# Optimization experiments

Hardware: AMD Instinct MI355X
Metric: run time of the kernel (lower is better)

## Reference

```python
import jax, jax.numpy as jnp
import numpy as np

HR, LR, K, RANK = 2048, 1024, 8, 16


def setup_inputs() -> dict:
    key = jax.random.key(0)
    kA, kX, kW, kU, kV, kM = jax.random.split(key, 6)
    A = jax.random.normal(kA, (LR, LR), dtype=jnp.float32)
    A = (A + A.T) / 2  # symmetric so torch UPLO='U' and jax eigh agree
    X = jax.random.normal(kX, (LR, HR), dtype=jnp.float32)
    init_range = (6.0 / (HR + HR)) ** 0.5  # glorot uniform
    weights = jax.random.uniform(kW, (HR, HR), dtype=jnp.float32,
                                 minval=-init_range, maxval=init_range)
    Us = jax.random.normal(kU, (K, HR, RANK), dtype=jnp.float32) * 0.001
    # original inits Vs to zeros; use small noise so corrections are nonzero
    Vs = jax.random.normal(kV, (K, HR, RANK), dtype=jnp.float32) * 0.01
    alphas = jnp.ones((K,), dtype=jnp.float32) / K
    masks = (jax.random.uniform(kM, (K, HR, HR)) < 0.5).astype(jnp.float32)
    return {"A": A, "X": X, "weights": weights, "Us": Us, "Vs": Vs,
            "alphas": alphas, "masks": masks}


def _set_unit_diag(M, eye):
    return M * (1.0 - eye) + eye


def reference(A, X, weights, Us, Vs, alphas, masks):
    lr = A.shape[0]
    hr = weights.shape[0]
    eye_hr = jnp.eye(hr, dtype=A.dtype)
    # --- GSRLayer ---
    _, U_lr = jnp.linalg.eigh(A)                      # (lr, lr)
    s_d = jnp.concatenate([jnp.eye(lr, dtype=A.dtype),
                           jnp.eye(lr, dtype=A.dtype)], axis=0)  # (hr, lr)
    f_d = weights @ s_d @ U_lr.T @ X                  # (hr, hr)
    adj = jnp.abs(f_d)
    adj = _set_unit_diag(adj, eye_hr)
    # --- community-aware low-rank corrections ---
    alpha = jax.nn.softmax(alphas)                    # (k,)
    Zm = adj[None, :, :] * masks                      # (k, hr, hr)
    t = jnp.einsum('kij,kjr->kir', Zm, Us)            # (k, hr, rank)
    corr = jnp.einsum('kir,kjr->kij', t, Vs) * masks  # (k, hr, hr)
    out_adj = adj + jnp.einsum('k,kij->ij', alpha, corr)
    # --- symmetrize with unit diagonal ---
    X_out = out_adj @ out_adj.T
    X_out = (X_out + X_out.T) / 2
    X_out = _set_unit_diag(X_out, eye_hr)
    return out_adj, jnp.abs(X_out)
```

## Files before the change

kernel.cpp:

```cpp
#include <hip/hip_runtime.h>
#include <hip/hip_bf16.h>

typedef unsigned long long u64;

#define MBYTE (1ull << 20)

static const size_t OFF_A64   = 0;
static const size_t OFF_VT    = 8*MBYTE;
static const size_t OFF_TAU   = 12*MBYTE;
static const size_t OFF_D64   = 12*MBYTE +  8192;
static const size_t OFF_E64   = 12*MBYTE + 16384;
static const size_t OFF_XB    = 12*MBYTE + 24576;
static const size_t OFF_Y2B   = 12*MBYTE + 32768;
static const size_t OFF_Y1B   = 12*MBYTE + 40960;
static const size_t OFF_XA    = 12*MBYTE + 49152;
static const size_t OFF_Y1A   = 12*MBYTE + 57344;
static const size_t OFF_Y2A   = 12*MBYTE + 65536;
static const size_t OFF_QA    = 13*MBYTE;
static const size_t OFF_QB    = 17*MBYTE;
static const size_t OFF_SHAT  = 21*MBYTE;
static const size_t OFF_WC    = 25*MBYTE;
static const size_t OFF_M1    = 33*MBYTE;
static const size_t OFF_T8    = 33*MBYTE;
static const size_t OFF_ALPHA = 35*MBYTE + 512*1024;
static const size_t OFF_ADJ   = 41*MBYTE;
static const size_t OFF_OADJ  = 17*MBYTE;
static const size_t OFF_CBUF  = 0;

static const size_t SCD_STRIDE = 9216;
static const size_t SCI_STRIDE = 6144;
static const size_t OFF_SCDB  = OFF_WC;
static const size_t OFF_SCIB  = OFF_WC + 2359296;
static const size_t OFF_KNB   = OFF_WC + 2359296 + 786432;
static const size_t OFF_KNDB  = OFF_WC + 2359296 + 786432 + 2048;


__global__ void kCopyA(const float* __restrict__ A, double* __restrict__ A64) {
  int gid = blockIdx.x*256 + threadIdx.x;
  if (gid < 1024*1024) A64[gid] = (double)A[gid];
}

__device__ __forceinline__ double agLoadD(const double* p) {
  return __hip_atomic_load(p, __ATOMIC_RELAXED, __HIP_MEMORY_SCOPE_AGENT);
}
__device__ __forceinline__ void agStoreD(double* p, double v) {
  __hip_atomic_store(p, v, __ATOMIC_RELAXED, __HIP_MEMORY_SCOPE_AGENT);
}

#define TD_NBLK 64

__global__ __launch_bounds__(1024) void kTriDiag(
    double* __restrict__ A64,
    double* __restrict__ y1A, double* __restrict__ y1B,
    double* __restrict__ y2A, double* __restrict__ y2B,
    double* __restrict__ diagP, unsigned* __restrict__ flags,
    double* __restrict__ tauv, double* __restrict__ e64, double* __restrict__ d64,
    float* __restrict__ Vt) {
  __shared__ double xL[1024], vL[1024], wL[1024], y1L[1024], y2L[1024];
  __shared__ double red[4];
  __shared__ double sS[4];
  int tid = threadIdx.x;
  int bid = blockIdx.x;
  bool w0 = (bid == 0);
  int lane = tid & 63, wave = tid >> 6;
  int myRow = wave*TD_NBLK + bid;

  double dg = 0.0;

  for (int i = 0; i <= 1023; ++i) {
    const double* y1in = (((i-1)&1) != 0) ? y1B : y1A;
    const double* y2in = (((i-1)&1) != 0) ? y2B : y2A;
    double* y1out = ((i&1) != 0) ? y1B : y1A;
    double* y2out = ((i&1) != 0) ? y2B : y2A;

    if (i == 0) {
      if (tid < 256) {
        for (int c = tid; c < 1024; c += 256) { vL[c] = 0.0; wL[c] = 0.0; }
        for (int c = 1 + tid; c < 1024; c += 256) xL[c] = A64[(u64)c*1024];
        if (w0 && tid == 0) d64[0] = A64[0];
      }
      __syncthreads();
    } else {
      int j = i - 1;
      double sy1 = agLoadD(&y1in[tid]);
      double sy2 = agLoadD(&y2in[tid]);
      if (w0 && tid == 0) dg = agLoadD(&diagP[i]);
      double acc = 0.0;
      if (tid < 256) {
        for (int c = i + 1 + tid; c < 1024; c += 256) { double v = xL[c]; acc += v*v; }
        for (int off = 32; off > 0; off >>= 1) acc += __shfl_xor(acc, off, 64);
      }
      y1L[tid] = sy1; y2L[tid] = sy2;
      if (tid < 256 && lane == 0) red[wave] = acc;
      __syncthreads();
      if (tid == 0) {
        double xn2 = red[0] + red[1] + red[2] + red[3];
        double alpha = xL[i];
        double tv, sc;
        if (xn2 == 0.0) { tv = 0.0; if (w0) e64[j] = alpha; sc = 0.0; }
        else {
          double beta = (alpha >= 0.0) ? -sqrt(alpha*alpha + xn2) : sqrt(alpha*alpha + xn2);
          tv = (beta - alpha)/beta;
          if (w0) e64[j] = beta;
          sc = 1.0/(alpha - beta);
        }
        if (w0) tauv[j] = tv;
        sS[0] = sc; sS[1] = tv;
        vL[i] = 1.0;
        if (w0) Vt[(u64)j*1024 + i] = 1.0f;
      }
      __syncthreads();
      if (tid < 256) {
        double sc = sS[0], tv = sS[1];
        double acc2 = 0.0;
        for (int r = i + tid; r < 1024; r += 256) {
          double v;
          if (r == i) v = 1.0;
          else {
            v = xL[r]*sc;
            vL[r] = v;
            if (w0) Vt[(u64)j*1024 + r] = (float)v;
          }
          double P = tv*(y1L[r] + sc*y2L[r]);
          wL[r] = P;
          acc2 += P*v;
        }
        for (int off = 32; off > 0; off >>= 1) acc2 += __shfl_xor(acc2, off, 64);
        if (lane == 0) red[wave] = acc2;
      }
      __syncthreads();
      if (tid == 0) {
        double coef = 0.5*sS[1]*(red[0] + red[1] + red[2] + red[3]);
        double wi = wL[i] - coef;
        sS[2] = coef; sS[3] = wi;
        if (w0) d64[i] = dg - 2.0*wi;
      }
      __syncthreads();
      if (tid < 256) {
        double coef = sS[2], wi = sS[3];
        for (int r = i + tid; r < 1024; r += 256) {
          double wcr = wL[r] - coef*vL[r];
          wL[r] = wcr;
          if (r > i) xL[r] = y1L[r] - vL[r]*wi - wcr;
        }
      }
      __syncthreads();
    }
    if (i <= 1022) {
      int r = myRow;
      if (r >= i + 1) {
        double vr = vL[r], wr = wL[r];
        double* Arow = A64 + (u64)r*1024;
        double acc = 0.0, y1v = 0.0;
        for (int c = i + 1 + lane; c < 1024; c += 64) {
          double a = Arow[c] - vr*wL[c] - wr*vL[c];
          Arow[c] = a;
          if (c == r) agStoreD(&diagP[r], a);
          if (c == i + 1) y1v = a; else acc += a*xL[c];
        }
        for (int off = 32; off > 0; off >>= 1) acc += __shfl_down(acc, off, 64);
        if (lane == 0) { agStoreD(&y1out[r], y1v); agStoreD(&y2out[r], acc); }
      }
      __syncthreads();
      unsigned tgt = (unsigned)(i + 1);
      if (tid == 0)
        __hip_atomic_store(&flags[bid*16], tgt, __ATOMIC_RELEASE, __HIP_MEMORY_SCOPE_AGENT);
      if (tid < TD_NBLK) {
        for (;;) {
          unsigned v = __hip_atomic_load(&flags[tid*16], __ATOMIC_ACQUIRE, __HIP_MEMORY_SCOPE_AGENT);
          if (__all(v >= tgt)) break;
          __builtin_amdgcn_s_sleep(2);
        }
      }
      __syncthreads();
    }
  }
  if (w0 && tid == 0) {
    for (int c = 16; c < 1024; c += 16) {
      double ae = fabs(e64[c-1]);
      d64[c-1] -= ae;
      d64[c]   -= ae;
    }
  }
}


__device__ void slartg_(double f, double g, double* cs, double* sn, double* r) {
  if (g == 0.0) { *cs = 1.0; *sn = 0.0; *r = f; }
  else if (f == 0.0) { *cs = 0.0; *sn = (g >= 0.0) ? 1.0 : -1.0; *r = fabs(g); }
  else {
    double d = sqrt(f*f + g*g);
    *cs = fabs(f)/d;
    *r = (f >= 0.0) ? d : -d;
    *sn = g / (*r);
  }
}

__device__ void slaev2_(double a, double b, double c, double* rt1, double* rt2,
                        double* cs1, double* sn1) {
  double sm = a + c, df = a - c, adf = fabs(df), tb = b + b, ab = fabs(tb);
  double acmx, acmn;
  if (fabs(a) > fabs(c)) { acmx = a; acmn = c; } else { acmx = c; acmn = a; }
  double rt;
  if (adf > ab) rt = adf*sqrt(1.0 + (ab/adf)*(ab/adf));
  else if (adf < ab) rt = ab*sqrt(1.0 + (adf/ab)*(adf/ab));
  else rt = ab*sqrt(2.0);
  int sgn1;
  if (sm < 0.0) { *rt1 = 0.5*(sm - rt); sgn1 = -1; *rt2 = (acmx / *rt1)*acmn - (b / *rt1)*b; }
  else if (sm > 0.0) { *rt1 = 0.5*(sm + rt); sgn1 = 1; *rt2 = (acmx / *rt1)*acmn - (b / *rt1)*b; }
  else { *rt1 = 0.5*rt; *rt2 = -0.5*rt; sgn1 = 1; }
  int sgn2; double cs;
  if (df >= 0.0) { cs = df + rt; sgn2 = 1; } else { cs = df - rt; sgn2 = -1; }
  double acs = fabs(cs);
  if (acs > ab) { double ct = -tb/cs; *sn1 = 1.0/sqrt(1.0 + ct*ct); *cs1 = ct*(*sn1); }
  else {
    if (ab == 0.0) { *cs1 = 1.0; *sn1 = 0.0; }
    else { double tn = -cs/tb; *cs1 = 1.0/sqrt(1.0 + tn*tn); *sn1 = tn*(*cs1); }
  }
  if (sgn1 == sgn2) { double tn = *cs1; *cs1 = -(*sn1); *sn1 = tn; }
}

__device__ void steqr16_(double* d, double* e, double* z, double* wc, double* ws_) {
  const int n = 16;
  const double eps = 5.9604644775390625e-08;
  const double eps2 = eps*eps;
  const double safmin = 1.1754943508222875e-38;
  int jtot = 0; const int nmaxit = n*30;
  int l1 = 0;
  for (int outer = 0; outer < 200; ++outer) {
    if (l1 > n-1) break;
    if (l1 > 0) e[l1-1] = 0.0;
    int m = l1;
    for (; m <= n-2; ++m) {
      double tst = fabs(e[m]);
      if (tst == 0.0) break;
      if (tst <= (sqrt(fabs(d[m]))*sqrt(fabs(d[m+1])))*eps) { e[m] = 0.0; break; }
    }
    int l = l1, lend = m;
    l1 = m + 1;
    if (lend == l) continue;
    if (fabs(d[lend]) < fabs(d[l])) { int t = l; l = lend; lend = t; }
    if (lend > l) {
      for (int it = 0; it < 800; ++it) {
        int mm = lend;
        if (l != lend) {
          for (mm = l; mm <= lend-1; ++mm) {
            double tst = e[mm]*e[mm];
            if (tst <= eps2*fabs(d[mm])*fabs(d[mm+1]) + safmin) break;
          }
        }
        if (mm < lend) e[mm] = 0.0;
        double p = d[l];
        if (mm == l) { d[l] = p; ++l; if (l <= lend) continue; break; }
        if (mm == l+1) {
          double rt1, rt2, c2, s2;
          slaev2_(d[l], e[l], d[l+1], &rt1, &rt2, &c2, &s2);
          for (int r = 0; r < n; ++r) {
            double t = z[r*16 + l + 1];
            z[r*16 + l + 1] = c2*t - s2*z[r*16 + l];
            z[r*16 + l]     = s2*t + c2*z[r*16 + l];
          }
          d[l] = rt1; d[l+1] = rt2; e[l] = 0.0;
          l += 2; if (l <= lend) continue; break;
        }
        if (jtot == nmaxit) break;
        ++jtot;
        double g = (d[l+1] - p)/(2.0*e[l]);
        double r_ = sqrt(g*g + 1.0);
        g = d[mm] - p + e[l]/(g + ((g >= 0.0) ? r_ : -r_));
        double s = 1.0, c = 1.0;
        p = 0.0;
        for (int i = mm-1; i >= l; --i) {
          double f = s*e[i], b = c*e[i];
          double cs, sn, rr;
          slartg_(g, f, &cs, &sn, &rr);
          c = cs; s = sn;
          if (i != mm-1) e[i+1] = rr;
          g = d[i+1] - p;
          rr = (d[i] - g)*s + 2.0*c*b;
          p = s*rr;
          d[i+1] = g + p;
          g = c*rr - b;
          wc[i] = c; ws_[i] = -s;
        }
        for (int jj = mm-1; jj >= l; --jj) {
          double cs = wc[jj], sn = ws_[jj];
          for (int r = 0; r < n; ++r) {
            double t = z[r*16 + jj + 1];
            z[r*16 + jj + 1] = cs*t - sn*z[r*16 + jj];
            z[r*16 + jj]     = sn*t + cs*z[r*16 + jj];
          }
        }
        d[l] -= p;
        e[l] = g;
      }
    } else {
      for (int it = 0; it < 800; ++it) {
        int mm = lend;
        if (l != lend) {
          for (mm = l; mm >= lend+1; --mm) {
            double tst = e[mm-1]*e[mm-1];
            if (tst <= eps2*fabs(d[mm])*fabs(d[mm-1]) + safmin) break;
          }
        }
        if (mm > lend) e[mm-1] = 0.0;
        double p = d[l];
        if (mm == l) { d[l] = p; --l; if (l >= lend) continue; break; }
        if (mm == l-1) {
          double rt1, rt2, c2, s2;
          slaev2_(d[l-1], e[l-1], d[l], &rt1, &rt2, &c2, &s2);
          for (int r = 0; r < n; ++r) {
            double t = z[r*16 + l];
            z[r*16 + l]     = c2*t - s2*z[r*16 + l - 1];
            z[r*16 + l - 1] = s2*t + c2*z[r*16 + l - 1];
          }
          d[l-1] = rt1; d[l] = rt2; e[l-1] = 0.0;
          l -= 2; if (l >= lend) continue; break;
        }
        if (jtot == nmaxit) break;
        ++jtot;
        double g = (d[l-1] - p)/(2.0*e[l-1]);
        double r_ = sqrt(g*g + 1.0);
        g = d[mm] - p + e[l-1]/(g + ((g >= 0.0) ? r_ : -r_));
        double s = 1.0, c = 1.0;
        p = 0.0;
        for (int i = mm; i <= l-1; ++i) {
          double f = s*e[i], b = c*e[i];
          double cs, sn, rr;
          slartg_(g, f, &cs, &sn, &rr);
          c = cs; s = sn;
          if (i != mm) e[i-1] = rr;
          g = d[i] - p;
          rr = (d[i+1] - g)*s + 2.0*c*b;
          p = s*rr;
          d[i] = g + p;
          g = c*rr - b;
          wc[i] = c; ws_[i] = s;
        }
        for (int jj = mm; jj <= l-1; ++jj) {
          double cs = wc[jj], sn = ws_[jj];
          for (int r = 0; r < n; ++r) {
            double t = z[r*16 + jj + 1];
            z[r*16 + jj + 1] = cs*t - sn*z[r*16 + jj];
            z[r*16 + jj]     = sn*t + cs*z[r*16 + jj];
          }
        }
        d[l] -= p;
        e[l-1] = g;
      }
    }
  }
  for (int ii = 1; ii <= n-1; ++ii) {
    int i = ii - 1, k = i;
    double p = d[i];
    for (int j = ii; j <= n-1; ++j) if (d[j] < p) { k = j; p = d[j]; }
    if (k != i) {
      d[k] = d[i]; d[i] = p;
      for (int r = 0; r < n; ++r) { double t = z[r*16 + i]; z[r*16 + i] = z[r*16 + k]; z[r*16 + k] = t; }
    }
  }
}

__global__ void kLeaf(double* d64, const double* e64, float* Qa) {
  __shared__ double dd[16], ed[16], zd[256], wk1[16], wk2[16];
  int leaf = blockIdx.x, lo = leaf*16, tid = threadIdx.x;
  for (int idx = tid; idx < 256; idx += 64) zd[idx] = ((idx/16) == (idx%16)) ? 1.0 : 0.0;
  if (tid < 16) { dd[tid] = d64[lo + tid]; ed[tid] = (tid < 15) ? e64[lo + tid] : 0.0; }
  __syncthreads();
  if (tid == 0) steqr16_(dd, ed, zd, wk1, wk2);
  __syncthreads();
  for (int idx = tid; idx < 256; idx += 64) {
    int r = idx/16, c = idx%16;
    Qa[(u64)(lo + r)*1024 + lo + c] = (float)zd[idx];
  }
  if (tid < 16) d64[lo + tid] = dd[tid];
}


__global__ __launch_bounds__(1024) void kDeflateB(float* __restrict__ Qa,
      const double* __restrict__ d64, const double* __restrict__ e64,
      double* scdB, int* sciB, int* knB, double* kndB, int bs) {
  __shared__ double zL[1024], dlocL[1024], redD[1024];
  __shared__ double rcL[1024], rsL[1024];
  __shared__ int sIdxL[1024], rpqL[1024];
  __shared__ double sSc[4];
  __shared__ int sKn[4];
  int mg = blockIdx.x;
  int n1 = bs, n = 2*bs, lo = mg*n;
  double* scd = scdB + (u64)mg*SCD_STRIDE;
  int*    sci = sciB + (u64)mg*SCI_STRIDE;
  int* kn = knB + mg*8;
  double* knd = kndB + mg*4;
  int tid = threadIdx.x;
  if (tid == 0) sSc[0] = e64[lo + n1 - 1];
  __syncthreads();
  double rho_in = sSc[0];
  const double invs2 = 0.70710678118654752440;
  if (tid < n) {
    int row = (tid < n1) ? (lo + n1 - 1) : (lo + n1);
    double s = (rho_in < 0.0 && tid >= n1) ? -invs2 : invs2;
    zL[tid] = (double)Qa[(u64)row*1024 + lo + tid] * s;
    dlocL[tid] = d64[lo + tid];
  }
  __syncthreads();
  if (tid < n) {
    int pos; double key = dlocL[tid];
    if (tid < n1) {
      int loB = 0, hiB = n - n1;
      while (loB < hiB) { int mid = (loB+hiB)>>1; if (dlocL[n1+mid] < key) loB = mid+1; else hiB = mid; }
      pos = tid + loB;
    } else {
      int loA = 0, hiA = n1;
      while (loA < hiA) { int mid = (loA+hiA)>>1; if (dlocL[mid] <= key) loA = mid+1; else hiA = mid; }
      pos = (tid - n1) + loA;
    }
    sIdxL[pos] = tid;
  }
  redD[tid] = (tid < n) ? fabs(zL[tid]) : 0.0;
  __syncthreads();
  for (int s = 512; s > 0; s >>= 1) { if (tid < s) redD[tid] = fmax(redD[tid], redD[tid+s]); __syncthreads(); }
  if (tid == 0) sSc[1] = redD[0];
  __syncthreads();
  redD[tid] = (tid < n) ? fabs(dlocL[tid]) : 0.0;
  __syncthreads();
  for (int s = 512; s > 0; s >>= 1) { if (tid < s) redD[tid] = fmax(redD[tid], redD[tid+s]); __syncthreads(); }
  if (tid == 0) {
    double zmax = sSc[1], dmax = redD[0];
    double rho = fabs(2.0*rho_in);
    double tol = 8.0*5.9604644775390625e-8*fmax(dmax, zmax);
    double* dlG = scd + 1024;
    double* wmG = scd + 2048;
    double* dvalG = scd + 7168;
    int* permG = sci;
    int* deflG = sci + 1024;
    int K = 0, nrot = 0, nd = 0; double sw2 = 0.0;
    if (rho*zmax <= tol) {
      for (int pos = 0; pos < n; ++pos) { int c = sIdxL[pos]; deflG[nd] = c; dvalG[nd] = dlocL[c]; nd++; }
    } else {
      int pj = -1, jpos = 0;
      for (; jpos < n; ++jpos) {
        int nj = sIdxL[jpos];
        if (rho*fabs(zL[nj]) <= tol) { deflG[nd] = nj; dvalG[nd] = dlocL[nj]; nd++; }
        else { pj = nj; break; }
      }
      for (++jpos; jpos < n; ++jpos) {
        int nj = sIdxL[jpos];
        if (rho*fabs(zL[nj]) <= tol) { deflG[nd] = nj; dvalG[nd] = dlocL[nj]; nd++; continue; }
        double s_ = zL[pj], c_ = zL[nj];
        double tu = sqrt(c_*c_ + s_*s_);
        double tdif = dlocL[nj] - dlocL[pj];
        c_ /= tu; s_ = -s_/tu;
        if (fabs(tdif*c_*s_) <= tol) {
          zL[nj] = tu; zL[pj] = 0.0;
          rpqL[nrot] = (pj << 16) | nj; rcL[nrot] = c_; rsL[nrot] = s_; nrot++;
          double t1 = dlocL[pj]*c_*c_ + dlocL[nj]*s_*s_;
          dlocL[nj] = dlocL[pj]*s_*s_ + dlocL[nj]*c_*c_;
          dlocL[pj] = t1;
          deflG[nd] = pj; dvalG[nd] = t1; nd++;
          pj = nj;
        } else {
          permG[K] = pj; dlG[K] = dlocL[pj]; wmG[K] = zL[pj]; sw2 += zL[pj]*zL[pj]; K++;
          pj = nj;
        }
      }
      permG[K] = pj; dlG[K] = dlocL[pj]; wmG[K] = zL[pj]; sw2 += zL[pj]*zL[pj]; K++;
    }
    sKn[1] = nrot;
    kn[0] = K; kn[1] = nrot; kn[2] = nd;
    knd[0] = rho; knd[1] = sw2;
  }
  __syncthreads();
  int nrot = sKn[1];
  if (tid < n && nrot > 0) {
    u64 row = (u64)(lo + tid)*1024;
    for (int t = 0; t < nrot; ++t) {
      int pq = rpqL[t];
      int p = lo + (pq >> 16), q = lo + (pq & 0xffff);
      double c = rcL[t], s = rsL[t];
      double x = (double)Qa[row + p], y = (double)Qa[row + q];
      Qa[row + p] = (float)(c*x + s*y);
      Qa[row + q] = (float)(c*y - s*x);
    }
  }
}

__global__ __launch_bounds__(256) void kSecularB(double* scdB, const int* knB, const double* kndB) {
  __shared__ double dlS[1024], wmS[1024];
  int mg = blockIdx.y;
  double* scd = scdB + (u64)mg*SCD_STRIDE;
  const int* kn = knB + mg*8;
  const double* knd = kndB + mg*4;
  int K = kn[0];
  int tid = threadIdx.x;
  for (int j = tid; j < K; j += 256) { dlS[j] = scd[1024 + j]; wmS[j] = scd[2048 + j]; }
  __syncthreads();
  int wave = tid >> 6, lane = tid & 63;
  int i = blockIdx.x*4 + wave;
  if (i >= K) return;
  double rho = knd[0], sw2 = knd[1];
  double di = dlS[i];
  double hi = (i < K-1) ? (dlS[i+1] - di) : (rho*sw2*(1.0 + 1e-12) + 1e-300);
  double lo_ = 0.0;
  for (int it = 0; it < 100; ++it) {
    double mid = 0.5*(lo_ + hi);
    double g = 0.0;
    for (int j = lane; j < K; j += 64) { double w = wmS[j]; g += w*w/((dlS[j] - di) - mid); }
    for (int off = 32; off > 0; off >>= 1) g += __shfl_xor(g, off);
    g = 1.0 + rho*g;
    if (g < 0.0) lo_ = mid; else hi = mid;
  }
  scd[3072 + i] = 0.5*(lo_ + hi);
}

__global__ void kZhatB(double* scdB, const int* knB) {
  int mg = blockIdx.y;
  double* scd = scdB + (u64)mg*SCD_STRIDE;
  int K = (knB + mg*8)[0];
  int j = blockIdx.x*64 + threadIdx.x;
  if (j >= K) return;
  const double* dl = scd + 1024;
  const double* wm = scd + 2048;
  const double* mu = scd + 3072;
  double dj = dl[j];
  double prod = mu[j];
  for (int i2 = 0; i2 < K; ++i2) {
    if (i2 == j) continue;
    double dd = dl[i2] - dj;
    prod *= (dd + mu[i2]) / dd;
  }
  prod = fabs(prod);
  scd[4096 + j] = (wm[j] >= 0.0) ? sqrt(prod) : -sqrt(prod);
}

__global__ __launch_bounds__(1024) void kSortPermB(double* scdB, int* sciB, const int* knB,
                                                   double* d64, int bs) {
  __shared__ double sv[1024];
  __shared__ int si[1024];
  int mg = blockIdx.x;
  int n = 2*bs, lo = mg*n;
  double* scd = scdB + (u64)mg*SCD_STRIDE;
  int* sci = sciB + (u64)mg*SCI_STRIDE;
  int K = (knB + mg*8)[0];
  int tid = threadIdx.x;
  const double* dl = scd + 1024;
  const double* mu = scd + 3072;
  const double* dval = scd + 7168;
  double v;
  if (tid < K) v = dl[tid] + mu[tid];
  else if (tid < n) v = dval[tid - K];
  else v = 1e300;
  sv[tid] = v; si[tid] = tid;
  __syncthreads();
  for (int k = 2; k <= 1024; k <<= 1) {
    for (int j = k >> 1; j > 0; j >>= 1) {
      int ixj = tid ^ j;
      if (ixj > tid) {
        bool up = ((tid & k) == 0);
        double a = sv[tid], b = sv[ixj];
        int ia = si[tid], ib = si[ixj];
        bool agtb = (a > b) || (a == b && ia > ib);
        if (up ? agtb : !agtb) { sv[tid] = b; sv[ixj] = a; si[tid] = ib; si[ixj] = ia; }
      }
      __syncthreads();
    }
  }
  if (tid < n) {
    int s = si[tid];
    if (s < K) sci[4096 + s] = tid; else sci[5120 + s - K] = tid;
    d64[lo + tid] = sv[tid];
  }
}

__global__ void kSvecNormB(float* __restrict__ Shat, const double* scdB, const int* knB, int bs) {
  int mg = blockIdx.y;
  int n = 2*bs, lo = mg*n;
  const double* scd = scdB + (u64)mg*SCD_STRIDE;
  int K = (knB + mg*8)[0];
  int i = blockIdx.x;
  if (i >= K) return;
  const double* dl = scd + 1024;
  const double* mu = scd + 3072;
  const double* zh = scd + 4096;
  __shared__ double red[256];
  int tid = threadIdx.x;
  double di = dl[i], m = mu[i];
  double acc = 0.0;
  for (int j = tid; j < K; j += 256) {
    double v = zh[j]/((dl[j] - di) - m);
    acc += v*v;
  }
  red[tid] = acc; __syncthreads();
  for (int s = 128; s > 0; s >>= 1) { if (tid < s) red[tid] += red[tid+s]; __syncthreads(); }
  double inv = 1.0/sqrt(red[0]);
  for (int j = tid; j < K; j += 256) {
    double v = zh[j]/((dl[j] - di) - m);
    Shat[(u64)j*1024 + lo + i] = (float)(v*inv);
  }
}

__global__ void kGatherB(const float* Qa, float* Qb, const int* sciB, const int* knB, int bs) {
  int mg = blockIdx.y;
  int n = 2*bs, lo = mg*n;
  const int* sci = sciB + (u64)mg*SCI_STRIDE;
  int K = (knB + mg*8)[0];
  int gid = blockIdx.x*256 + threadIdx.x;
  if (gid >= n*n) return;
  int p = gid % n, r = gid / n;
  int src = (p < K) ? sci[p] : sci[1024 + p - K];
  Qb[(u64)(lo + r)*1024 + p] = Qa[(u64)(lo + r)*1024 + lo + src];
}

__global__ void kGemmMergeB(const float* __restrict__ Qb, const float* __restrict__ Shat,
                            float* __restrict__ Qa, const int* sciB, const int* knB, int bs) {
  __shared__ float As[16][17], Bs[16][17];
  int mg = blockIdx.z;
  int n = 2*bs, lo = mg*n;
  const int* sci = sciB + (u64)mg*SCI_STRIDE;
  int K = (knB + mg*8)[0];
  int tx = threadIdx.x, ty = threadIdx.y;
  int r0 = blockIdx.y*16, c0 = blockIdx.x*16;
  const int* rootpos = sci + 4096;
  float acc = 0.f;
  for (int k0 = 0; k0 < K; k0 += 16) {
    As[ty][tx] = (k0 + tx < K) ? Qb[(u64)(lo + r0 + ty)*1024 + k0 + tx] : 0.f;
    Bs[ty][tx] = (k0 + ty < K && c0 + tx < K) ? Shat[(u64)(k0 + ty)*1024 + lo + c0 + tx] : 0.f;
    __syncthreads();
    #pragma unroll
    for (int kk = 0; kk < 16; ++kk) acc += As[ty][kk]*Bs[kk][tx];
    __syncthreads();
  }
  int i = c0 + tx;
  if (i < K) Qa[(u64)(lo + r0 + ty)*1024 + lo + rootpos[i]] = acc;
}

__global__ void kScatterDeflB(const float* Qb, float* Qa, const int* sciB, const int* knB, int bs) {
  int mg = blockIdx.y;
  int n = 2*bs, lo = mg*n;
  const int* sci = sciB + (u64)mg*SCI_STRIDE;
  const int* kn = knB + mg*8;
  int gid = blockIdx.x*256 + threadIdx.x;
  if (gid >= n*n) return;
  int p = gid % n, r = gid / n;
  int K = kn[0], nd = kn[2];
  if (p < K || p - K >= nd) return;
  Qa[(u64)(lo + r)*1024 + lo + sci[5120 + p - K]] = Qb[(u64)(lo + r)*1024 + p];
}

__global__ void kBackx(float* __restrict__ Qa, const float* __restrict__ Vt,
                       const double* __restrict__ tau) {
  __shared__ double redA[256], redB[256], redS[16];
  __shared__ double fA[16], fB[16];
  int tid = threadIdx.x;
  int cix = tid & 15, strip = tid >> 4;
  int col = blockIdx.x*16 + cix;
  for (int a = 1022; a >= 2; a -= 2) {
    int b = a - 1;
    double ta = tau[a], tb = tau[b];
    const float* va_row = Vt + (u64)a*1024;
    const float* vb_row = Vt + (u64)b*1024;
    double pda = 0.0, pdb = 0.0, ps = 0.0;
    for (int r = a + strip; r < 1024; r += 16) {
      double zb = (double)Qa[(u64)r*1024 + col];
      double va = (r > a) ? (double)va_row[r] : 0.0;
      double vb = (double)vb_row[r];
      pda += va*zb; pdb += vb*zb;
      if (cix == 0) ps += va*vb;
    }
    redA[tid] = pda; redB[tid] = pdb;
    if (cix == 0) redS[strip] = ps;
    __syncthreads();
    if (tid < 16) {
      double da = 0.0, db = 0.0, s = 0.0;
      for (int u = 0; u < 16; ++u) {
        da += redA[u*16 + tid];
        db += redB[u*16 + tid];
        s  += redS[u];
      }
      fA[tid] = ta*da;
      fB[tid] = tb*(db - ta*s*da);
    }
    __syncthreads();
    double fa = fA[cix], fb = fB[cix];
    for (int r = a + strip; r < 1024; r += 16) {
      double va = (r > a) ? (double)va_row[r] : 0.0;
      double vb = (double)vb_row[r];
      Qa[(u64)r*1024 + col] -= (float)(fa*va + fb*vb);
    }
    __syncthreads();
  }
  {
    double t0 = tau[0];
    const float* v_row = Vt;
    double pd = 0.0;
    for (int r = 1 + strip; r < 1024; r += 16)
      pd += (double)v_row[r] * (double)Qa[(u64)r*1024 + col];
    redA[tid] = pd;
    __syncthreads();
    if (tid < 16) {
      double d = 0.0;
      for (int u = 0; u < 16; ++u) d += redA[u*16 + tid];
      fA[tid] = t0*d;
    }
    __syncthreads();
    double f = fA[cix];
    for (int r = 1 + strip; r < 1024; r += 16)
      Qa[(u64)r*1024 + col] -= (float)(f * (double)v_row[r]);
  }
}


template<int TA, int TB>
__global__ __launch_bounds__(256) void gemm_f32(const float* __restrict__ A,
    const float* __restrict__ B, float* __restrict__ C,
    int M, int N, int Kd, int lda, int ldb, int ldc) {
  __shared__ float As[8][132];
  __shared__ float Bs[8][132];
  int tid = threadIdx.x;
  int bi = blockIdx.y*128, bj = blockIdx.x*128;
  int tx = tid & 15, ty = tid >> 4;
  float acc[8][8];
  #pragma unroll
  for (int x = 0; x < 8; ++x)
    #pragma unroll
    for (int y = 0; y < 8; ++y) acc[x][y] = 0.f;
  for (int k0 = 0; k0 < Kd; k0 += 8) {
    if (TA == 0) {
      int row = tid >> 1, kc = (tid & 1)*4;
      float4 v = *(const float4*)&A[(u64)(bi + row)*lda + k0 + kc];
      As[kc+0][row] = v.x; As[kc+1][row] = v.y; As[kc+2][row] = v.z; As[kc+3][row] = v.w;
    } else {
      int kk = tid >> 5, col = (tid & 31)*4;
      float4 v = *(const float4*)&A[(u64)(k0 + kk)*lda + bi + col];
      *(float4*)&As[kk][col] = v;
    }
    if (TB == 0) {
      int kk = tid >> 5, col = (tid & 31)*4;
      float4 v = *(const float4*)&B[(u64)(k0 + kk)*ldb + bj + col];
      *(float4*)&Bs[kk][col] = v;
    } else {
      int row = tid >> 1, kc = (tid & 1)*4;
      float4 v = *(const float4*)&B[(u64)(bj + row)*ldb + k0 + kc];
      Bs[kc+0][row] = v.x; Bs[kc+1][row] = v.y; Bs[kc+2][row] = v.z; Bs[kc+3][row] = v.w;
    }
    __syncthreads();
    #pragma unroll
    for (int kk = 0; kk < 8; ++kk) {
      float a[8], b[8];
      *(float4*)&a[0] = *(float4*)&As[kk][ty*8];
      *(float4*)&a[4] = *(float4*)&As[kk][ty*8 + 4];
      *(float4*)&b[0] = *(float4*)&Bs[kk][tx*8];
      *(float4*)&b[4] = *(float4*)&Bs[kk][tx*8 + 4];
      #pragma unroll
      for (int x = 0; x < 8; ++x)
        #pragma unroll
        for (int y = 0; y < 8; ++y) acc[x][y] += a[x]*b[y];
    }
    __syncthreads();
  }
  #pragma unroll
  for (int x = 0; x < 8; ++x) {
    float* Crow = &C[(u64)(bi + ty*8 + x)*ldc + bj + tx*8];
    *(float4*)&Crow[0] = make_float4(acc[x][0], acc[x][1], acc[x][2], acc[x][3]);
    *(float4*)&Crow[4] = make_float4(acc[x][4], acc[x][5], acc[x][6], acc[x][7]);
  }
}

__global__ void kWc(const float* W, float* Wc) {
  int gid = blockIdx.x*256 + threadIdx.x;
  if (gid >= 2048*1024) return;
  int i = gid >> 10, k = gid & 1023;
  Wc[gid] = W[(u64)i*2048 + k] + W[(u64)i*2048 + 1024 + k];
}

__global__ void kAbsDiag(float* adj) {
  int gid = blockIdx.x*256 + threadIdx.x;
  if (gid >= 2048*2048) return;
  int i = gid >> 11, j = gid & 2047;
  float v = fabsf(adj[gid]);
  adj[gid] = (i == j) ? 1.0f : v;
}

__global__ void kTk(const float* __restrict__ adj, const float* __restrict__ masks,
                    const float* __restrict__ Us, float* __restrict__ t8) {
  int k = blockIdx.y;
  int i = blockIdx.x*16 + (threadIdx.x >> 4);
  int r = threadIdx.x & 15;
  const float* arow = adj + (u64)i*2048;
  const float* mrow = masks + ((u64)k*2048 + i)*2048;
  const float* uk = Us + (u64)k*2048*16 + r;
  float acc = 0.f;
  for (int j = 0; j < 2048; ++j) acc += arow[j]*mrow[j]*uk[(u64)j*16];
  t8[((u64)k*2048 + i)*16 + r] = acc;
}

__global__ void kAlpha(const float* alphas, float* alpha) {
  if (threadIdx.x == 0 && blockIdx.x == 0) {
    float m = alphas[0];
    for (int k = 1; k < 8; ++k) m = fmaxf(m, alphas[k]);
    float e[8]; float s = 0.f;
    for (int k = 0; k < 8; ++k) { e[k] = expf(alphas[k] - m); s += e[k]; }
    for (int k = 0; k < 8; ++k) alpha[k] = e[k]/s;
  }
}

__global__ void kOutAdj(const float* __restrict__ adj, const float* __restrict__ masks,
                        const float* __restrict__ Vs, const float* __restrict__ t8,
                        const float* __restrict__ alpha, float* __restrict__ oadj,
                        float* __restrict__ out0) {
  __shared__ float tS[8][16][16];
  __shared__ float vS[8][16][16];
  int j0 = blockIdx.x*16, i0 = blockIdx.y*16;
  int tid = threadIdx.x;
  for (int idx = tid; idx < 2048; idx += 256) {
    int k = idx >> 8, rem = idx & 255, row = rem >> 4, r = rem & 15;
    tS[k][row][r] = t8[((u64)k*2048 + i0 + row)*16 + r];
    vS[k][row][r] = Vs[((u64)k*2048 + j0 + row)*16 + r];
  }
  __syncthreads();
  int ii = tid >> 4, jj = tid & 15;
  int i = i0 + ii, j = j0 + jj;
  float corr = 0.f;
  for (int k = 0; k < 8; ++k) {
    float m = masks[((u64)k*2048 + i)*2048 + j];
    float dv = 0.f;
    #pragma unroll
    for (int r = 0; r < 16; ++r) dv += tS[k][ii][r]*vS[k][jj][r];
    corr += alpha[k]*m*dv;
  }
  float val = adj[(u64)i*2048 + j] + corr;
  oadj[(u64)i*2048 + j] = val;
  out0[(u64)i*2048 + j] = val;
}

__global__ void kFinal(const float* __restrict__ C, float* __restrict__ out1) {
  int gid = blockIdx.x*256 + threadIdx.x;
  if (gid >= 2048*2048) return;
  int i = gid >> 11, j = gid & 2047;
  float v;
  if (i == j) v = 1.0f;
  else v = 0.5f*(C[gid] + C[(u64)j*2048 + i]);
  out1[gid] = fabsf(v);
}


extern "C" void kernel_launch(void* const* d_in, const int* in_sizes, int n_in,
                              void* d_out, int out_size, void* d_ws, size_t ws_size,
                              hipStream_t stream) {
  const float* A      = (const float*)d_in[0];
  const float* X      = (const float*)d_in[1];
  const float* W      = (const float*)d_in[2];
  const float* Us     = (const float*)d_in[3];
  const float* Vs     = (const float*)d_in[4];
  const float* alphas = (const float*)d_in[5];
  const float* masks  = (const float*)d_in[6];

  char* ws = (char*)d_ws;
  double* A64  = (double*)(ws + OFF_A64);
  float*  Vt   = (float*) (ws + OFF_VT);
  double* tau  = (double*)(ws + OFF_TAU);
  double* d64  = (double*)(ws + OFF_D64);
  double* e64  = (double*)(ws + OFF_E64);
  double* diagP = (double*)(ws + OFF_XA);
  unsigned* flags = (unsigned*)(ws + OFF_XB);
  double* y1a  = (double*)(ws + OFF_Y1A);
  double* y1b  = (double*)(ws + OFF_Y1B);
  double* y2a  = (double*)(ws + OFF_Y2A);
  double* y2b  = (double*)(ws + OFF_Y2B);
  double* SCDB = (double*)(ws + OFF_SCDB);
  int*    SCIB = (int*)   (ws + OFF_SCIB);
  int*    KNB  = (int*)   (ws + OFF_KNB);
  double* KNDB = (double*)(ws + OFF_KNDB);
  float*  ALPH = (float*) (ws + OFF_ALPHA);
  float*  Qa   = (float*) (ws + OFF_QA);
  float*  Qb   = (float*) (ws + OFF_QB);
  float*  Shat = (float*) (ws + OFF_SHAT);
  float*  Wc   = (float*) (ws + OFF_WC);
  float*  M1   = (float*) (ws + OFF_M1);
  float*  T8   = (float*) (ws + OFF_T8);
  float*  ADJ  = (float*) (ws + OFF_ADJ);
  float*  OADJ = (float*) (ws + OFF_OADJ);
  float*  CB   = (float*) (ws + OFF_CBUF);

  float* out0 = (float*)d_out;
  float* out1 = out0 + (u64)2048*2048;

  hipMemsetAsync(ws + OFF_XB, 0, 4096, stream);
  kCopyA<<<4096, 256, 0, stream>>>(A, A64);
  {
    void* kargs[] = { (void*)&A64, (void*)&y1a, (void*)&y1b, (void*)&y2a, (void*)&y2b,
                      (void*)&diagP, (void*)&flags,
                      (void*)&tau, (void*)&e64, (void*)&d64, (void*)&Vt };
    hipLaunchCooperativeKernel((void*)kTriDiag, dim3(TD_NBLK), dim3(1024), kargs, 0, stream);
  }

  hipMemsetAsync(Qa, 0, (size_t)4*MBYTE, stream);
  kLeaf<<<64, 64, 0, stream>>>(d64, e64, Qa);

  for (int lvl = 0; lvl < 6; ++lvl) {
    int bs = 16 << lvl;
    int n = 2*bs;
    int cnt = 1024/n;
    kDeflateB<<<cnt, 1024, 0, stream>>>(Qa, d64, e64, SCDB, SCIB, KNB, KNDB, bs);
    kSecularB<<<dim3((n + 3)/4, cnt), 256, 0, stream>>>(SCDB, KNB, KNDB);
    kZhatB<<<dim3((n + 63)/64, cnt), 64, 0, stream>>>(SCDB, KNB);
    kSortPermB<<<cnt, 1024, 0, stream>>>(SCDB, SCIB, KNB, d64, bs);
    kSvecNormB<<<dim3(n, cnt), 256, 0, stream>>>(Shat, SCDB, KNB, bs);
    kGatherB<<<dim3((n*n + 255)/256, cnt), 256, 0, stream>>>(Qa, Qb, SCIB, KNB, bs);
    kGemmMergeB<<<dim3(n/16, n/16, cnt), dim3(16, 16), 0, stream>>>(Qb, Shat, Qa, SCIB, KNB, bs);
    kScatterDeflB<<<dim3((n*n + 255)/256, cnt), 256, 0, stream>>>(Qb, Qa, SCIB, KNB, bs);
  }

  kBackx<<<64, 256, 0, stream>>>(Qa, Vt, tau);

  kWc<<<8192, 256, 0, stream>>>(W, Wc);
  gemm_f32<1,0><<<dim3(16, 8), 256, 0, stream>>>(Qa, X, M1, 1024, 2048, 1024, 1024, 2048, 2048);
  gemm_f32<0,0><<<dim3(16, 16), 256, 0, stream>>>(Wc, M1, ADJ, 2048, 2048, 1024, 1024, 2048, 2048);
  kAbsDiag<<<16384, 256, 0, stream>>>(ADJ);
  kTk<<<dim3(128, 8), 256, 0, stream>>>(ADJ, masks, Us, T8);
  kAlpha<<<1, 64, 0, stream>>>(alphas, ALPH);
  kOutAdj<<<dim3(128, 128), 256, 0, stream>>>(ADJ, masks, Vs, T8, ALPH, OADJ, out0);
  gemm_f32<0,1><<<dim3(16, 16), 256, 0, stream>>>(OADJ, OADJ, CB, 2048, 2048, 2048, 2048, 2048, 2048);
  kFinal<<<16384, 256, 0, stream>>>(CB, out1);
}
```

Baseline: 20.27 ms.

## Apply Householder back-transformation with blocked WY compact form

Replaces the sequential two-reflector-at-a-time back-transformation kernel, which ran in 64 blocks with many barriers per reflector pair, with a blocked compact-WY scheme. Each panel of 64 reflectors builds W = V^T Q and the Gram matrix, forms the triangular T factor, then applies Q -= V (T W) as a tiled GEMM-like update. Vt is first zeroed on and below the diagonal so the reflectors can be read as dense panels. The aim is more parallelism and data reuse, at the cost of about 16 iterations of three kernel launches, extra workspace, and a serial T-factor build inside each panel.

```diff
diff --git a/kernel.cpp b/kernel.cpp
--- a/kernel.cpp
+++ b/kernel.cpp
@@ -34,6 +34,10 @@
 static const size_t OFF_KNB   = OFF_WC + 2359296 + 786432;
 static const size_t OFF_KNDB  = OFF_WC + 2359296 + 786432 + 2048;
 
+static const size_t OFF_WYW   = OFF_WC;
+static const size_t OFF_WYTW  = OFF_WC + 524288;
+static const size_t OFF_WYG   = OFF_WC + 1048576;
+
 
 __global__ void kCopyA(const float* __restrict__ A, double* __restrict__ A64) {
   int gid = blockIdx.x*256 + threadIdx.x;
@@ -646,65 +650,171 @@
   Qa[(u64)(lo + r)*1024 + lo + sci[5120 + p - K]] = Qb[(u64)(lo + r)*1024 + p];
 }
 
-__global__ void kBackx(float* __restrict__ Qa, const float* __restrict__ Vt,
-                       const double* __restrict__ tau) {
-  __shared__ double redA[256], redB[256], redS[16];
-  __shared__ double fA[16], fB[16];
+
+__global__ void kVtZero(float* __restrict__ Vt) {
+  int gid = blockIdx.x*256 + threadIdx.x;
+  if (gid >= 1024*1024) return;
+  int row = gid >> 10, col = gid & 1023;
+  if (col <= row) Vt[gid] = 0.f;
+}
+
+__global__ __launch_bounds__(256) void kWyW(const float* __restrict__ Vt,
+    const float* __restrict__ Qa, double* __restrict__ W, double* __restrict__ G,
+    int i0, int rbeg) {
+  __shared__ float sA[64][33];
+  __shared__ float sB[32][65];
   int tid = threadIdx.x;
-  int cix = tid & 15, strip = tid >> 4;
-  int col = blockIdx.x*16 + cix;
-  for (int a = 1022; a >= 2; a -= 2) {
-    int b = a - 1;
-    double ta = tau[a], tb = tau[b];
-    const float* va_row = Vt + (u64)a*1024;
-    const float* vb_row = Vt + (u64)b*1024;
-    double pda = 0.0, pdb = 0.0, ps = 0.0;
-    for (int r = a + strip; r < 1024; r += 16) {
-      double zb = (double)Qa[(u64)r*1024 + col];
-      double va = (r > a) ? (double)va_row[r] : 0.0;
-      double vb = (double)vb_row[r];
-      pda += va*zb; pdb += vb*zb;
-      if (cix == 0) ps += va*vb;
-    }
-    redA[tid] = pda; redB[tid] = pdb;
-    if (cix == 0) redS[strip] = ps;
+  int tx = tid & 15, ty = tid >> 4;
+  if (blockIdx.x < 16) {
+    int c0 = blockIdx.x*64;
+    double acc[4][4];
+    #pragma unroll
+    for (int i = 0; i < 4; ++i)
+      #pragma unroll
+      for (int k = 0; k < 4; ++k) acc[i][k] = 0.0;
+    for (int r0 = rbeg; r0 < 1024; r0 += 32) {
+      #pragma unroll
+      for (int k = 0; k < 8; ++k) {
+        int e = tid + k*256;
+        int j = e >> 5, rr = e & 31;
+        int r = r0 + rr;
+        sA[j][rr] = (r < 1024) ? Vt[(u64)(i0 + j)*1024 + r] : 0.f;
+      }
+      #pragma unroll
+      for (int k = 0; k < 8; ++k) {
+        int e = tid + k*256;
+        int rr = e >> 6, cc = e & 63;
+        int r = r0 + rr;
+        sB[rr][cc] = (r < 1024) ? Qa[(u64)r*1024 + c0 + cc] : 0.f;
+      }
+      __syncthreads();
+      for (int rr = 0; rr < 32; ++rr) {
+        double a0 = sA[ty*4+0][rr], a1 = sA[ty*4+1][rr];
+        double a2 = sA[ty*4+2][rr], a3 = sA[ty*4+3][rr];
+        double b0 = sB[rr][tx*4+0], b1 = sB[rr][tx*4+1];
+        double b2 = sB[rr][tx*4+2], b3 = sB[rr][tx*4+3];
+        acc[0][0] += a0*b0; acc[0][1] += a0*b1; acc[0][2] += a0*b2; acc[0][3] += a0*b3;
+        acc[1][0] += a1*b0; acc[1][1] += a1*b1; acc[1][2] += a1*b2; acc[1][3] += a1*b3;
+        acc[2][0] += a2*b0; acc[2][1] += a2*b1; acc[2][2] += a2*b2; acc[2][3] += a2*b3;
+        acc[3][0] += a3*b0; acc[3][1] += a3*b1; acc[3][2] += a3*b2; acc[3][3] += a3*b3;
+      }
+      __syncthreads();
+    }
+    #pragma unroll
+    for (int i = 0; i < 4; ++i)
+      #pragma unroll
+      for (int k = 0; k < 4; ++k)
+        W[(u64)(ty*4+i)*1024 + c0 + tx*4 + k] = acc[i][k];
+  } else {
+    double acc[16];
+    #pragma unroll
+    for (int k = 0; k < 16; ++k) acc[k] = 0.0;
+    for (int r0 = rbeg; r0 < 1024; r0 += 32) {
+      #pragma unroll
+      for (int k = 0; k < 8; ++k) {
+        int e = tid + k*256;
+        int j = e >> 5, rr = e & 31;
+        int r = r0 + rr;
+        sA[j][rr] = (r < 1024) ? Vt[(u64)(i0 + j)*1024 + r] : 0.f;
+      }
+      __syncthreads();
+      #pragma unroll
+      for (int k = 0; k < 16; ++k) {
+        int e = tid + k*256;
+        int j1 = e >> 6, j2 = e & 63;
+        double s = acc[k];
+        for (int rr = 0; rr < 32; ++rr) s += (double)sA[j1][rr]*(double)sA[j2][rr];
+        acc[k] = s;
+      }
+      __syncthreads();
+    }
+    #pragma unroll
+    for (int k = 0; k < 16; ++k) {
+      int e = tid + k*256;
+      G[(e >> 6)*64 + (e & 63)] = acc[k];
+    }
+  }
+}
+
+__global__ __launch_bounds__(256) void kWyT(const double* __restrict__ G,
+    const double* __restrict__ tau, const double* __restrict__ W,
+    double* __restrict__ TW, int i0, int nbk) {
+  __shared__ double sT[64][65];
+  int tid = threadIdx.x;
+  for (int e = tid; e < 64*65; e += 256) (&sT[0][0])[e] = 0.0;
+  __syncthreads();
+  if (tid < nbk) sT[tid][tid] = tau[i0 + tid];
+  __syncthreads();
+  for (int m = 1; m < nbk; ++m) {
+    if (tid < m) {
+      double s = 0.0;
+      for (int q = tid; q < m; ++q) s += sT[tid][q]*G[q*64 + m];
+      sT[tid][m] = -tau[i0 + m]*s;
+    }
     __syncthreads();
-    if (tid < 16) {
-      double da = 0.0, db = 0.0, s = 0.0;
-      for (int u = 0; u < 16; ++u) {
-        da += redA[u*16 + tid];
-        db += redB[u*16 + tid];
-        s  += redS[u];
-      }
-      fA[tid] = ta*da;
-      fB[tid] = tb*(db - ta*s*da);
-    }
-    __syncthreads();
-    double fa = fA[cix], fb = fB[cix];
-    for (int r = a + strip; r < 1024; r += 16) {
-      double va = (r > a) ? (double)va_row[r] : 0.0;
-      double vb = (double)vb_row[r];
-      Qa[(u64)r*1024 + col] -= (float)(fa*va + fb*vb);
-    }
-    __syncthreads();
-  }
-  {
-    double t0 = tau[0];
-    const float* v_row = Vt;
-    double pd = 0.0;
-    for (int r = 1 + strip; r < 1024; r += 16)
-      pd += (double)v_row[r] * (double)Qa[(u64)r*1024 + col];
-    redA[tid] = pd;
-    __syncthreads();
-    if (tid < 16) {
-      double d = 0.0;
-      for (int u = 0; u < 16; ++u) d += redA[u*16 + tid];
-      fA[tid] = t0*d;
-    }
-    __syncthreads();
-    double f = fA[cix];
-    for (int r = 1 + strip; r < 1024; r += 16)
-      Qa[(u64)r*1024 + col] -= (float)(f * (double)v_row[r]);
+  }
+  int tx = tid & 15, ty = tid >> 4;
+  int c0 = blockIdx.x*64;
+  #pragma unroll
+  for (int i = 0; i < 4; ++i) {
+    int j = ty*4 + i;
+    #pragma unroll
+    for (int k = 0; k < 4; ++k) {
+      int c = c0 + tx*4 + k;
+      double s = 0.0;
+      for (int q = j; q < 64; ++q) s += sT[j][q]*W[(u64)q*1024 + c];
+      TW[(u64)j*1024 + c] = s;
+    }
+  }
+}
+
+__global__ __launch_bounds__(256) void kWyU(const float* __restrict__ Vt,
+    const double* __restrict__ TW, float* __restrict__ Qa, int i0, int rbeg) {
+  __shared__ float sV[64][65];
+  __shared__ double sTW[64][65];
+  int tid = threadIdx.x;
+  int r0 = rbeg + blockIdx.x*64;
+  int c0 = blockIdx.y*64;
+  #pragma unroll
+  for (int k = 0; k < 16; ++k) {
+    int e = tid + k*256;
+    int j = e >> 6, rr = e & 63;
+    int r = r0 + rr;
+    sV[rr][j] = (r < 1024) ? Vt[(u64)(i0 + j)*1024 + r] : 0.f;
+  }
+  #pragma unroll
+  for (int k = 0; k < 16; ++k) {
+    int e = tid + k*256;
+    int j = e >> 6, cc = e & 63;
+    sTW[j][cc] = TW[(u64)j*1024 + c0 + cc];
+  }
+  __syncthreads();
+  int tx = tid & 15, ty = tid >> 4;
+  double acc[4][4];
+  #pragma unroll
+  for (int i = 0; i < 4; ++i)
+    #pragma unroll
+    for (int k = 0; k < 4; ++k) acc[i][k] = 0.0;
+  for (int j = 0; j < 64; ++j) {
+    double v0 = sV[ty*4+0][j], v1 = sV[ty*4+1][j];
+    double v2 = sV[ty*4+2][j], v3 = sV[ty*4+3][j];
+    double t0 = sTW[j][tx*4+0], t1 = sTW[j][tx*4+1];
+    double t2 = sTW[j][tx*4+2], t3 = sTW[j][tx*4+3];
+    acc[0][0] += v0*t0; acc[0][1] += v0*t1; acc[0][2] += v0*t2; acc[0][3] += v0*t3;
+    acc[1][0] += v1*t0; acc[1][1] += v1*t1; acc[1][2] += v1*t2; acc[1][3] += v1*t3;
+    acc[2][0] += v2*t0; acc[2][1] += v2*t1; acc[2][2] += v2*t2; acc[2][3] += v2*t3;
+    acc[3][0] += v3*t0; acc[3][1] += v3*t1; acc[3][2] += v3*t2; acc[3][3] += v3*t3;
+  }
+  #pragma unroll
+  for (int i = 0; i < 4; ++i) {
+    int r = r0 + ty*4 + i;
+    if (r < 1024) {
+      #pragma unroll
+      for (int k = 0; k < 4; ++k) {
+        u64 a = (u64)r*1024 + c0 + tx*4 + k;
+        Qa[a] = (float)((double)Qa[a] - acc[i][k]);
+      }
+    }
   }
 }
 
@@ -870,6 +980,9 @@
   int*    SCIB = (int*)   (ws + OFF_SCIB);
   int*    KNB  = (int*)   (ws + OFF_KNB);
   double* KNDB = (double*)(ws + OFF_KNDB);
+  double* WYW  = (double*)(ws + OFF_WYW);
+  double* WYTW = (double*)(ws + OFF_WYTW);
+  double* WYG  = (double*)(ws + OFF_WYG);
   float*  ALPH = (float*) (ws + OFF_ALPHA);
   float*  Qa   = (float*) (ws + OFF_QA);
   float*  Qb   = (float*) (ws + OFF_QB);
@@ -910,7 +1023,15 @@
     kScatterDeflB<<<dim3((n*n + 255)/256, cnt), 256, 0, stream>>>(Qb, Qa, SCIB, KNB, bs);
   }
 
-  kBackx<<<64, 256, 0, stream>>>(Qa, Vt, tau);
+  kVtZero<<<4096, 256, 0, stream>>>(Vt);
+  for (int i0 = 960; i0 >= 0; i0 -= 64) {
+    int nbk = (i0 == 960) ? 63 : 64;
+    int rbeg = i0 + 1;
+    int L = 1024 - rbeg;
+    kWyW<<<17, 256, 0, stream>>>(Vt, Qa, WYW, WYG, i0, rbeg);
+    kWyT<<<16, 256, 0, stream>>>(WYG, tau, WYW, WYTW, i0, nbk);
+    kWyU<<<dim3((L + 63)/64, 16), 256, 0, stream>>>(Vt, WYTW, Qa, i0, rbeg);
+  }
 
   kWc<<<8192, 256, 0, stream>>>(W, Wc);
   gemm_f32<1,0><<<dim3(16, 8), 256, 0, stream>>>(Qa, X, M1, 1024, 2048, 1024, 1024, 2048, 2048);
```

New measurement: 16.78 ms. 17.2% less time.
